# Kernel optimization log

Measured on AMD Instinct MI355X. Metric: run time of the kernel, lower is better.

## Reference

```python
import jax, jax.numpy as jnp
import numpy as np

N_HEAD = 16
EPS = 1e-6


def setup_inputs() -> dict:
    key = jax.random.key(0)
    ks = jax.random.split(key, 5)
    B, T, C = 2, 2048, 1024
    hd = C // N_HEAD
    x = jax.random.normal(ks[0], (B, T, C), dtype=jnp.float32)
    # rotary frequencies (unit-magnitude complex, decomposed into cos/sin)
    theta = 10000.0 ** (-np.arange(0, hd, 2, dtype=np.float32) / hd)  # [hd/2]
    ang = np.arange(T, dtype=np.float32)[:, None] * theta[None, :]    # [T, hd/2]
    freqs_cos = jnp.asarray(np.cos(ang))
    freqs_sin = jnp.asarray(np.sin(ang))
    w_attn = jax.random.normal(ks[1], (3 * C, C), dtype=jnp.float32) * 0.02
    w_proj = jax.random.normal(ks[2], (C, C), dtype=jnp.float32) * 0.02
    q_norm_w = jnp.ones((hd,), dtype=jnp.float32)
    k_norm_w = jnp.ones((hd,), dtype=jnp.float32)
    return {"x": x, "freqs_cos": freqs_cos, "freqs_sin": freqs_sin,
            "w_attn": w_attn, "w_proj": w_proj,
            "q_norm_w": q_norm_w, "k_norm_w": k_norm_w}


def _rmsnorm(x, w):
    # x: [..., hd]; per-last-dim RMSNorm with learned scale
    rms = jax.lax.rsqrt(jnp.mean(x * x, axis=-1, keepdims=True) + EPS)
    return x * rms * w


def _rope(x, cos, sin):
    # x: [B, T, H, hd]; cos/sin: [T, hd/2] -> broadcast [1, T, 1, hd/2]
    x2 = x.reshape(*x.shape[:-1], -1, 2)  # [B,T,H,hd/2,2]
    x0, x1 = x2[..., 0], x2[..., 1]
    c = cos[None, :, None, :]
    s = sin[None, :, None, :]
    r0 = x0 * c - x1 * s
    r1 = x0 * s + x1 * c
    return jnp.stack([r0, r1], axis=-1).reshape(x.shape)


def reference(x, freqs_cos, freqs_sin, w_attn, w_proj, q_norm_w, k_norm_w):
    B, T, C = x.shape
    H = N_HEAD
    hd = C // H
    qkv = x @ w_attn.T  # [B, T, 3C]
    q, k, v = jnp.split(qkv, 3, axis=-1)
    q = q.reshape(B, T, H, hd)
    k = k.reshape(B, T, H, hd)
    v = v.reshape(B, T, H, hd)
    q = _rmsnorm(q, q_norm_w)
    k = _rmsnorm(k, k_norm_w)
    q = _rope(q, freqs_cos[:T], freqs_sin[:T])
    k = _rope(k, freqs_cos[:T], freqs_sin[:T])
    scale = 1.0 / jnp.sqrt(jnp.asarray(hd, dtype=x.dtype))
    # causal SDPA: scores [B, H, T, T]
    scores = jnp.einsum('bihd,bjhd->bhij', q, k) * scale
    causal = jnp.tril(jnp.ones((T, T), dtype=bool))
    scores = jnp.where(causal[None, None], scores, jnp.finfo(scores.dtype).min)
    p = jax.nn.softmax(scores, axis=-1)
    y = jnp.einsum('bhij,bjhd->bihd', p, v).reshape(B, T, C)
    return y @ w_proj.T
```

## Files before the change

kernel.cpp:

```cpp
#include <hip/hip_runtime.h>

typedef unsigned short u16;
typedef unsigned int u32;
typedef __bf16 bf16x8 __attribute__((ext_vector_type(8)));
typedef float f32x4 __attribute__((ext_vector_type(4)));

__device__ __forceinline__ u16 f2bf(float f) {
    union { float f; u32 u; } v;
    v.f = f;
    u32 r = v.u + 0x7fffu + ((v.u >> 16) & 1u);
    return (u16)(r >> 16);
}

__device__ __forceinline__ u32 fbits(float f) {
    union { float f; u32 u; } v; v.f = f; return v.u;
}

__device__ __forceinline__ void glds16(const void* g, void* l) {
    __builtin_amdgcn_global_load_lds(
        (__attribute__((address_space(1))) unsigned int*)(g),
        (__attribute__((address_space(3))) unsigned int*)(l), 16, 0, 0);
}

#define MFMA __builtin_amdgcn_mfma_f32_16x16x32_bf16

__global__ void castbf3(const float* __restrict__ a, u16* __restrict__ oa,
                        const float* __restrict__ b, u16* __restrict__ ob,
                        const float* __restrict__ c, u16* __restrict__ oc,
                        const float* __restrict__ fcos, const float* __restrict__ fsin,
                        float2* __restrict__ csb) {
    int blk = blockIdx.x;
    if (blk < 4096) {
        int i = blk * 256 + threadIdx.x;
        float4 v = ((const float4*)a)[i];
        ushort4 o;
        o.x = f2bf(v.x); o.y = f2bf(v.y); o.z = f2bf(v.z); o.w = f2bf(v.w);
        ((ushort4*)oa)[i] = o;
    } else if (blk < 7168) {
        int i = (blk - 4096) * 256 + threadIdx.x;
        int n = i >> 8, c4 = i & 255;
        int np;
        if (n < 2048) {
            int part = n >> 10, rem = n & 1023;
            int h = rem >> 6, d = rem & 63;
            int nd = (d >> 1) + ((d & 1) << 5);
            np = part * 1024 + h * 64 + nd;
        } else np = n;
        float4 v = ((const float4*)b)[i];
        ushort4 o;
        o.x = f2bf(v.x); o.y = f2bf(v.y); o.z = f2bf(v.z); o.w = f2bf(v.w);
        ((ushort4*)ob)[np * 256 + c4] = o;
    } else if (blk < 8192) {
        int i = (blk - 7168) * 256 + threadIdx.x;
        float4 v = ((const float4*)c)[i];
        ushort4 o;
        o.x = f2bf(v.x); o.y = f2bf(v.y); o.z = f2bf(v.z); o.w = f2bf(v.w);
        ((ushort4*)oc)[i] = o;
    } else {
        int i = (blk - 8192) * 256 + threadIdx.x;
        csb[i] = make_float2(fcos[i], fsin[i]);
    }
}

__global__ __launch_bounds__(256) void gemm_qkv(
    const u16* __restrict__ A, const u16* __restrict__ B,
    const float2* __restrict__ csb,
    const float* __restrict__ qw, const float* __restrict__ kw,
    u16* __restrict__ q, u16* __restrict__ k, u16* __restrict__ vt)
{
    __shared__ alignas(16) u16 SB[2 * 8192];
    u16* Es = SB;
    const int tid = threadIdx.x;
    const int lane = tid & 63;
    const int wave = tid >> 6;
    const int bm = blockIdx.y * 128, bn = blockIdx.x * 128;
    const int wm = (wave >> 1) * 64, wn = (wave & 1) * 64;
    const int ln = lane & 15, quad = lane >> 4;
    const int K = 1024;

    f32x4 acc[4][4] = {};

    const int srow = tid >> 2;
    const int scol = (tid & 3) * 8;
    const u16* gA = A + (size_t)(bm + srow) * K + scol;
    const u16* gB = B + (size_t)(bn + srow) * K + scol;

    auto stage = [&](int k0, int bf) {
        u16* lA = &SB[bf * 8192 + wave * 512];
        u16* lB = &SB[bf * 8192 + 4096 + wave * 512];
        glds16(gA + k0, lA);
        glds16(gA + (size_t)64 * K + k0, lA + 2048);
        glds16(gB + k0, lB);
        glds16(gB + (size_t)64 * K + k0, lB + 2048);
    };

    stage(0, 0);
    for (int it = 0; it < 32; ++it) {
        stage((((it + 1) & 31) << 5), (it + 1) & 1);
        asm volatile("s_waitcnt vmcnt(4)\n\ts_barrier" ::: "memory");

        const u16* Asb = &SB[(it & 1) * 8192];
        const u16* Bsb = Asb + 4096;
        bf16x8 af[4], bfr[4];
#pragma unroll
        for (int i = 0; i < 4; ++i)
            af[i] = *(const bf16x8*)&Asb[(wm + i * 16 + ln) * 32 + quad * 8];
#pragma unroll
        for (int j = 0; j < 4; ++j)
            bfr[j] = *(const bf16x8*)&Bsb[(wn + j * 16 + ln) * 32 + quad * 8];
#pragma unroll
        for (int i = 0; i < 4; ++i)
#pragma unroll
            for (int j = 0; j < 4; ++j)
                acc[i][j] = MFMA(af[i], bfr[j], acc[i][j], 0, 0, 0);

        asm volatile("s_barrier" ::: "memory");
    }
    asm volatile("s_waitcnt vmcnt(0)\n\ts_barrier" ::: "memory");

    const int part = bn >> 10;
    const int headw = wave & 1;
    const int h0 = (bn & 1023) >> 6;
    const float SC = 0.18033688011112042f;
    const int b = bm >> 11, tbase = bm & 2047;

    if (part == 2) {
#pragma unroll
        for (int i = 0; i < 4; ++i) {
            int tlb = wm + i * 16 + quad * 4;
#pragma unroll
            for (int j = 0; j < 4; ++j) {
                int d = j * 16 + ln;
                uint2 pk;
                pk.x = __builtin_amdgcn_perm(fbits(acc[i][j][1]), fbits(acc[i][j][0]), 0x07060302u);
                pk.y = __builtin_amdgcn_perm(fbits(acc[i][j][3]), fbits(acc[i][j][2]), 0x07060302u);
                *(uint2*)&Es[headw * 8192 + d * 128 + (tlb ^ (ln << 3))] = pk;
            }
        }
        __syncthreads();
#pragma unroll
        for (int c = 0; c < 8; ++c) {
            int cid = c * 256 + tid;
            int tc = cid & 15, d = (cid >> 4) & 63, hd = cid >> 10;
            uint4 v = *(const uint4*)&Es[hd * 8192 + d * 128 + ((tc ^ (d & 15)) << 3)];
            size_t dst = ((size_t)((b * 16 + h0 + hd) * 64 + d)) * 2048
                       + tbase + ((tc >> 3) << 6) + (((tc & 7) ^ (d & 7)) << 3);
            *(uint4*)&vt[dst] = v;
        }
        return;
    }

    const float* nw = (part == 0) ? qw : kw;
    float wv[4];
#pragma unroll
    for (int j = 0; j < 4; ++j) {
        int nd = j * 16 + ln;
        int od = ((nd & 31) << 1) | (nd >> 5);
        wv[j] = nw[od];
    }

    if (part == 0) {
#pragma unroll
        for (int i = 0; i < 4; ++i) {
            float oj[4][4];
#pragma unroll
            for (int r = 0; r < 4; ++r) {
                int tloc = wm + i * 16 + quad * 4 + r;
                int t = (bm + tloc) & 2047;
                float v0 = acc[i][0][r], v1 = acc[i][1][r];
                float v2 = acc[i][2][r], v3 = acc[i][3][r];
                float ss = v0 * v0 + v1 * v1 + v2 * v2 + v3 * v3;
                ss += __shfl_xor(ss, 1);
                ss += __shfl_xor(ss, 2);
                ss += __shfl_xor(ss, 4);
                ss += __shfl_xor(ss, 8);
                float g = rsqrtf(ss * (1.0f / 64.0f) + 1e-6f) * SC;
                float x0a = v0 * g * wv[0], x0b = v1 * g * wv[1];
                float x1a = v2 * g * wv[2], x1b = v3 * g * wv[3];
                float2 cs0 = csb[t * 32 + ln];
                float2 cs1 = csb[t * 32 + 16 + ln];
                oj[0][r] = x0a * cs0.x - x1a * cs0.y;
                oj[2][r] = x0a * cs0.y + x1a * cs0.x;
                oj[1][r] = x0b * cs1.x - x1b * cs1.y;
                oj[3][r] = x0b * cs1.y + x1b * cs1.x;
            }
            int tlb = wm + i * 16 + quad * 4;
#pragma unroll
            for (int j = 0; j < 4; ++j) {
                uint2 pk;
                pk.x = __builtin_amdgcn_perm(fbits(oj[j][1]), fbits(oj[j][0]), 0x07060302u);
                pk.y = __builtin_amdgcn_perm(fbits(oj[j][3]), fbits(oj[j][2]), 0x07060302u);
                *(uint2*)&Es[headw * 8192 + (j * 16 + ln) * 128 + (tlb ^ (ln << 3))] = pk;
            }
        }
        __syncthreads();
#pragma unroll
        for (int c = 0; c < 8; ++c) {
            int cid = c * 256 + tid;
            int tc = cid & 15, d = (cid >> 4) & 63, hd = cid >> 10;
            uint4 v = *(const uint4*)&Es[hd * 8192 + d * 128 + ((tc ^ (d & 15)) << 3)];
            size_t dst = ((size_t)((b * 16 + h0 + hd) * 64 + d)) * 2048 + tbase + tc * 8;
            *(uint4*)&q[dst] = v;
        }
        return;
    }

#pragma unroll
    for (int i = 0; i < 4; ++i) {
#pragma unroll
        for (int r = 0; r < 4; ++r) {
            int tloc = wm + i * 16 + quad * 4 + r;
            int t = (bm + tloc) & 2047;

            float v0 = acc[i][0][r], v1 = acc[i][1][r];
            float v2 = acc[i][2][r], v3 = acc[i][3][r];
            float ss = v0 * v0 + v1 * v1 + v2 * v2 + v3 * v3;
            ss += __shfl_xor(ss, 1);
            ss += __shfl_xor(ss, 2);
            ss += __shfl_xor(ss, 4);
            ss += __shfl_xor(ss, 8);
            float g = rsqrtf(ss * (1.0f / 64.0f) + 1e-6f);

            float x0a = v0 * g * wv[0], x0b = v1 * g * wv[1];
            float x1a = v2 * g * wv[2], x1b = v3 * g * wv[3];
            float2 cs0 = csb[t * 32 + ln];
            float2 cs1 = csb[t * 32 + 16 + ln];
            float o0 = x0a * cs0.x - x1a * cs0.y;
            float o2 = x0a * cs0.y + x1a * cs0.x;
            float o1 = x0b * cs1.x - x1b * cs1.y;
            float o3 = x0b * cs1.y + x1b * cs1.x;

            u16* e = &Es[headw * 8192 + tloc * 64 + ln];
            e[((0 ^ quad) << 4)] = f2bf(o0);
            e[((1 ^ quad) << 4)] = f2bf(o1);
            e[((2 ^ quad) << 4)] = f2bf(o2);
            e[((3 ^ quad) << 4)] = f2bf(o3);
        }
    }
    __syncthreads();
#pragma unroll
    for (int c = 0; c < 8; ++c) {
        int cid = c * 256 + tid;
        int dc = cid & 7, tloc = (cid >> 3) & 127, hd = cid >> 10;
        int q2 = (tloc >> 2) & 3;
        int sq = (dc >> 1) ^ q2;
        uint4 v = *(const uint4*)&Es[hd * 8192 + tloc * 64 + sq * 16 + (dc & 1) * 8];
        int gm = bm + tloc;
        int bb = gm >> 11, t = gm & 2047;
        size_t rb = ((size_t)((bb * 16 + h0 + hd) * 2048 + t)) * 64;
        *(uint4*)&k[rb + ((dc ^ (t & 7)) << 3)] = v;
    }
}

__global__ __launch_bounds__(256) void gemm64(
    const u16* __restrict__ A, const u16* __restrict__ B,
    float* __restrict__ C, int M, int N, int K)
{
    __shared__ alignas(16) u16 SB[2 * 6144];
    const int tid = threadIdx.x;
    const int lane = tid & 63;
    const int wave = tid >> 6;
    const int bm = blockIdx.y * 64, bn = blockIdx.x * 128;
    const int wm = (wave >> 1) * 32, wn = (wave & 1) * 64;
    const int ln = lane & 15, quad = lane >> 4;

    f32x4 acc[2][4] = {};

    const int srow = tid >> 2;
    const int scol = (tid & 3) * 8;
    const u16* gA = A + (size_t)(bm + srow) * K + scol;
    const u16* gB = B + (size_t)(bn + srow) * K + scol;

    auto stage = [&](int k0, int bf) {
        u16* lA = &SB[bf * 6144 + wave * 512];
        u16* lB = &SB[bf * 6144 + 2048 + wave * 512];
        glds16(gA + k0, lA);
        glds16(gB + k0, lB);
        glds16(gB + (size_t)64 * K + k0, lB + 2048);
    };

    stage(0, 0);
    for (int it = 0; it < 32; ++it) {
        stage((((it + 1) & 31) << 5), (it + 1) & 1);
        asm volatile("s_waitcnt vmcnt(3)\n\ts_barrier" ::: "memory");

        const u16* Asb = &SB[(it & 1) * 6144];
        const u16* Bsb = Asb + 2048;
        bf16x8 af[2], bfr[4];
#pragma unroll
        for (int i = 0; i < 2; ++i)
            af[i] = *(const bf16x8*)&Asb[(wm + i * 16 + ln) * 32 + quad * 8];
#pragma unroll
        for (int j = 0; j < 4; ++j)
            bfr[j] = *(const bf16x8*)&Bsb[(wn + j * 16 + ln) * 32 + quad * 8];
#pragma unroll
        for (int i = 0; i < 2; ++i)
#pragma unroll
            for (int j = 0; j < 4; ++j)
                acc[i][j] = MFMA(af[i], bfr[j], acc[i][j], 0, 0, 0);

        asm volatile("s_barrier" ::: "memory");
    }

#pragma unroll
    for (int i = 0; i < 2; ++i) {
#pragma unroll
        for (int r = 0; r < 4; ++r) {
            int gm = bm + wm + i * 16 + quad * 4 + r;
            float* Crow = C + (size_t)gm * N + bn + wn + ln;
#pragma unroll
            for (int j = 0; j < 4; ++j)
                Crow[j * 16] = acc[i][j][r];
        }
    }
}

__global__ __launch_bounds__(512) void attn_kernel(
    const u16* __restrict__ Q, const u16* __restrict__ K,
    const u16* __restrict__ VT, u16* __restrict__ Y)
{
    __shared__ alignas(16) u16 Ks[2][64 * 64];
    __shared__ alignas(16) u16 Vs[2][64 * 64];
    __shared__ alignas(16) u16 Ps[8][16 * 80];

    const int tid = threadIdx.x;
    const int lane = tid & 63;
    const int wave = tid >> 6;
    const int ln = lane & 15, quad = lane >> 4;
    const int pi = blockIdx.x;
    const int bh = blockIdx.y;
    const int qaIdx = pi, qbIdx = 31 - pi;
    const bool isB = wave >= 4;
    const int qidx = isB ? qbIdx : qaIdx;
    const int myq = qidx * 64 + (wave & 3) * 16;
    const size_t base = (size_t)bh * 2048 * 64;
    const u16* Kg = K + base;
    const u16* Vg = VT + base;
    const __bf16* Qg = (const __bf16*)(Q + base);

    const int qt = myq + ln;
    bf16x8 qf0, qf1;
#pragma unroll
    for (int j = 0; j < 8; ++j) {
        qf0[j] = Qg[(size_t)(quad * 8 + j) * 2048 + qt];
        qf1[j] = Qg[(size_t)(32 + quad * 8 + j) * 2048 + qt];
    }

    f32x4 o[4] = {};
    float l = 0.0f;
    const int nstages = qbIdx + 1;
    const int sw = ln & 7;
    const int srow = wave * 8 + (lane >> 3);
    const int scol = (lane & 7) * 8;
    u16* Psw = &Ps[wave][0];

    auto prefetch = [&](int jb, int nb) {
        glds16(&Kg[(size_t)(jb + srow) * 64 + scol], &Ks[nb][wave * 512]);
        glds16(&Vg[(size_t)srow * 2048 + jb + scol], &Vs[nb][wave * 512]);
    };
    auto computeS = [&](f32x4* st, const u16* ksb) {
#pragma unroll
        for (int ct = 0; ct < 4; ++ct) {
            bf16x8 kf0 = *(const bf16x8*)&ksb[(ct * 16 + ln) * 64 + (quad ^ sw) * 8];
            bf16x8 kf1 = *(const bf16x8*)&ksb[(ct * 16 + ln) * 64 + ((4 + quad) ^ sw) * 8];
            f32x4 z = {};
            z = MFMA(kf0, qf0, z, 0, 0, 0);
            st[ct] = MFMA(kf1, qf1, z, 0, 0, 0);
        }
    };
    auto applyMask = [&](f32x4* st, int jb) {
        const int qg = myq + ln;
#pragma unroll
        for (int ct = 0; ct < 4; ++ct)
#pragma unroll
            for (int r = 0; r < 4; ++r)
                if (jb + ct * 16 + quad * 4 + r > qg) st[ct][r] = -1e30f;
    };

    prefetch(0, 0);
    asm volatile("s_waitcnt vmcnt(0)\n\ts_barrier" ::: "memory");
    f32x4 st[4];
    computeS(st, &Ks[0][0]);
    if (qidx == 0) applyMask(st, 0);

    for (int jt = 0; jt < nstages; ++jt) {
        const bool haveNext = (jt + 1 < nstages);
        if (haveNext) prefetch((jt + 1) * 64, (jt + 1) & 1);

        const bool curActive = isB || jt <= qaIdx;
        if (curActive) {
            float sum = 0.0f;
#pragma unroll
            for (int ct = 0; ct < 4; ++ct) {
                float e0 = exp2f(st[ct][0]), e1 = exp2f(st[ct][1]);
                float e2 = exp2f(st[ct][2]), e3 = exp2f(st[ct][3]);
                sum += (e0 + e1) + (e2 + e3);
                uint2 pk;
                pk.x = __builtin_amdgcn_perm(fbits(e1), fbits(e0), 0x07060302u);
                pk.y = __builtin_amdgcn_perm(fbits(e3), fbits(e2), 0x07060302u);
                *(uint2*)&Psw[ln * 80 + ct * 16 + quad * 4] = pk;
            }
            l += sum;
        }

        asm volatile("s_waitcnt vmcnt(0)\n\ts_barrier" ::: "memory");

        const bool nextActive = haveNext && (isB || (jt + 1) <= qaIdx);
        if (nextActive) {
            computeS(st, &Ks[(jt + 1) & 1][0]);
            if (jt + 1 == qidx) applyMask(st, (jt + 1) * 64);
        }

        if (curActive) {
            __builtin_amdgcn_s_waitcnt(0xC07F);
            bf16x8 pf0 = *(const bf16x8*)&Psw[ln * 80 + quad * 8];
            bf16x8 pf1 = *(const bf16x8*)&Psw[ln * 80 + 32 + quad * 8];
            const u16* vsb = &Vs[jt & 1][0];
#pragma unroll
            for (int dt = 0; dt < 4; ++dt) {
                bf16x8 vf0 = *(const bf16x8*)&vsb[(dt * 16 + ln) * 64 + (quad ^ sw) * 8];
                bf16x8 vf1 = *(const bf16x8*)&vsb[(dt * 16 + ln) * 64 + ((4 + quad) ^ sw) * 8];
                o[dt] = MFMA(pf0, vf0, o[dt], 0, 0, 0);
                o[dt] = MFMA(pf1, vf1, o[dt], 0, 0, 0);
            }
        }
        asm volatile("s_waitcnt lgkmcnt(0)\n\ts_barrier" ::: "memory");
    }

    l += __shfl_xor(l, 16);
    l += __shfl_xor(l, 32);

    const int b = bh >> 4, h = bh & 15;
#pragma unroll
    for (int r = 0; r < 4; ++r) {
        float lr = __shfl(l, (lane & 48) + quad * 4 + r);
        float inv = 1.0f / lr;
        int gq = myq + quad * 4 + r;
        size_t yb = ((size_t)(b * 2048 + gq)) * 1024 + h * 64 + ln;
#pragma unroll
        for (int dt = 0; dt < 4; ++dt)
            Y[yb + dt * 16] = f2bf(o[dt][r] * inv);
    }
}

extern "C" void kernel_launch(void* const* d_in, const int* in_sizes, int n_in,
                              void* d_out, int out_size, void* d_ws, size_t ws_size,
                              hipStream_t stream) {
    const float* x      = (const float*)d_in[0];
    const float* fcos   = (const float*)d_in[1];
    const float* fsin   = (const float*)d_in[2];
    const float* w_attn = (const float*)d_in[3];
    const float* w_proj = (const float*)d_in[4];
    const float* qw     = (const float*)d_in[5];
    const float* kw     = (const float*)d_in[6];
    float* out = (float*)d_out;

    char* ws = (char*)d_ws;
    u16*    xb  = (u16*)(ws + 0);
    u16*    yb  = (u16*)(ws + 0);
    u16*    wab = (u16*)(ws + 8388608);
    u16*    wpb = (u16*)(ws + 14680064);
    u16*    qb  = (u16*)(ws + 16777216);
    u16*    kb  = (u16*)(ws + 25165824);
    u16*    vtb = (u16*)(ws + 33554432);
    float2* csb = (float2*)(ws + 41943040);

    castbf3<<<8448, 256, 0, stream>>>(x, xb, w_attn, wab, w_proj, wpb, fcos, fsin, csb);

    gemm_qkv<<<dim3(24, 32), 256, 0, stream>>>(xb, wab, csb, qw, kw, qb, kb, vtb);

    attn_kernel<<<dim3(16, 32), 512, 0, stream>>>(qb, kb, vtb, yb);

    gemm64<<<dim3(8, 64), 256, 0, stream>>>(yb, wpb, out, 4096, 1024, 1024);
}
```

Measured before the change: 187.6 us.

## Give each attention wave two 16-row query tiles, halve block size, add setprio

The attention block shrinks from 8 to 4 waves, and each wave now handles 32 query rows as two 16-row sub-tiles. Each K and V fragment read from LDS is therefore reused across two MFMA sets, which halves LDS fragment traffic per unit of compute. Each wave now issues four global-to-LDS loads per stage instead of two. The MFMA sections are wrapped in s_setprio to favour matrix issue. Costs are higher register pressure (doubled accumulators, scores and Q fragments) and fewer waves per block to hide latency.

Measured after the change: 213.2 us. 13.7% more time.

```diff
diff --git a/kernel.cpp b/kernel.cpp
--- a/kernel.cpp
+++ b/kernel.cpp
@@ -315,13 +315,13 @@
     }
 }
 
-__global__ __launch_bounds__(512) void attn_kernel(
+__global__ __launch_bounds__(256) void attn_kernel(
     const u16* __restrict__ Q, const u16* __restrict__ K,
     const u16* __restrict__ VT, u16* __restrict__ Y)
 {
     __shared__ alignas(16) u16 Ks[2][64 * 64];
     __shared__ alignas(16) u16 Vs[2][64 * 64];
-    __shared__ alignas(16) u16 Ps[8][16 * 80];
+    __shared__ alignas(16) u16 Ps[4][2][16 * 80];
 
     const int tid = threadIdx.x;
     const int lane = tid & 63;
@@ -330,58 +330,69 @@
     const int pi = blockIdx.x;
     const int bh = blockIdx.y;
     const int qaIdx = pi, qbIdx = 31 - pi;
-    const bool isB = wave >= 4;
+    const bool isB = wave >= 2;
     const int qidx = isB ? qbIdx : qaIdx;
-    const int myq = qidx * 64 + (wave & 3) * 16;
+    const int myq = qidx * 64 + (wave & 1) * 32;
     const size_t base = (size_t)bh * 2048 * 64;
     const u16* Kg = K + base;
     const u16* Vg = VT + base;
     const __bf16* Qg = (const __bf16*)(Q + base);
 
-    const int qt = myq + ln;
-    bf16x8 qf0, qf1;
-#pragma unroll
-    for (int j = 0; j < 8; ++j) {
-        qf0[j] = Qg[(size_t)(quad * 8 + j) * 2048 + qt];
-        qf1[j] = Qg[(size_t)(32 + quad * 8 + j) * 2048 + qt];
-    }
-
-    f32x4 o[4] = {};
-    float l = 0.0f;
+    bf16x8 qf[2][2];
+#pragma unroll
+    for (int m = 0; m < 2; ++m) {
+        const int qt = myq + m * 16 + ln;
+#pragma unroll
+        for (int j = 0; j < 8; ++j) {
+            qf[m][0][j] = Qg[(size_t)(quad * 8 + j) * 2048 + qt];
+            qf[m][1][j] = Qg[(size_t)(32 + quad * 8 + j) * 2048 + qt];
+        }
+    }
+
+    f32x4 o[2][4] = {};
+    float l[2] = {0.0f, 0.0f};
     const int nstages = qbIdx + 1;
     const int sw = ln & 7;
-    const int srow = wave * 8 + (lane >> 3);
-    const int scol = (lane & 7) * 8;
-    u16* Psw = &Ps[wave][0];
+    const int r8 = lane >> 3;
+    const int c8 = (lane & 7) * 8;
 
     auto prefetch = [&](int jb, int nb) {
-        glds16(&Kg[(size_t)(jb + srow) * 64 + scol], &Ks[nb][wave * 512]);
-        glds16(&Vg[(size_t)srow * 2048 + jb + scol], &Vs[nb][wave * 512]);
+        glds16(&Kg[(size_t)(jb + wave * 16 + r8) * 64 + c8], &Ks[nb][wave * 1024]);
+        glds16(&Kg[(size_t)(jb + wave * 16 + 8 + r8) * 64 + c8], &Ks[nb][wave * 1024 + 512]);
+        glds16(&Vg[(size_t)(wave * 16 + r8) * 2048 + jb + c8], &Vs[nb][wave * 1024]);
+        glds16(&Vg[(size_t)(wave * 16 + 8 + r8) * 2048 + jb + c8], &Vs[nb][wave * 1024 + 512]);
     };
-    auto computeS = [&](f32x4* st, const u16* ksb) {
+
+    f32x4 st[2][4];
+    auto computeS = [&](const u16* ksb) {
 #pragma unroll
         for (int ct = 0; ct < 4; ++ct) {
             bf16x8 kf0 = *(const bf16x8*)&ksb[(ct * 16 + ln) * 64 + (quad ^ sw) * 8];
             bf16x8 kf1 = *(const bf16x8*)&ksb[(ct * 16 + ln) * 64 + ((4 + quad) ^ sw) * 8];
-            f32x4 z = {};
-            z = MFMA(kf0, qf0, z, 0, 0, 0);
-            st[ct] = MFMA(kf1, qf1, z, 0, 0, 0);
+#pragma unroll
+            for (int m = 0; m < 2; ++m) {
+                f32x4 z = {};
+                z = MFMA(kf0, qf[m][0], z, 0, 0, 0);
+                st[m][ct] = MFMA(kf1, qf[m][1], z, 0, 0, 0);
+            }
         }
     };
-    auto applyMask = [&](f32x4* st, int jb) {
-        const int qg = myq + ln;
-#pragma unroll
-        for (int ct = 0; ct < 4; ++ct)
-#pragma unroll
-            for (int r = 0; r < 4; ++r)
-                if (jb + ct * 16 + quad * 4 + r > qg) st[ct][r] = -1e30f;
+    auto applyMask = [&](int jb) {
+#pragma unroll
+        for (int m = 0; m < 2; ++m) {
+            const int qg = myq + m * 16 + ln;
+#pragma unroll
+            for (int ct = 0; ct < 4; ++ct)
+#pragma unroll
+                for (int r = 0; r < 4; ++r)
+                    if (jb + ct * 16 + quad * 4 + r > qg) st[m][ct][r] = -1e30f;
+        }
     };
 
     prefetch(0, 0);
     asm volatile("s_waitcnt vmcnt(0)\n\ts_barrier" ::: "memory");
-    f32x4 st[4];
-    computeS(st, &Ks[0][0]);
-    if (qidx == 0) applyMask(st, 0);
+    computeS(&Ks[0][0]);
+    if (qidx == 0) applyMask(0);
 
     for (int jt = 0; jt < nstages; ++jt) {
         const bool haveNext = (jt + 1 < nstages);
@@ -389,57 +400,75 @@
 
         const bool curActive = isB || jt <= qaIdx;
         if (curActive) {
-            float sum = 0.0f;
-#pragma unroll
-            for (int ct = 0; ct < 4; ++ct) {
-                float e0 = exp2f(st[ct][0]), e1 = exp2f(st[ct][1]);
-                float e2 = exp2f(st[ct][2]), e3 = exp2f(st[ct][3]);
-                sum += (e0 + e1) + (e2 + e3);
-                uint2 pk;
-                pk.x = __builtin_amdgcn_perm(fbits(e1), fbits(e0), 0x07060302u);
-                pk.y = __builtin_amdgcn_perm(fbits(e3), fbits(e2), 0x07060302u);
-                *(uint2*)&Psw[ln * 80 + ct * 16 + quad * 4] = pk;
-            }
-            l += sum;
+#pragma unroll
+            for (int m = 0; m < 2; ++m) {
+                float sum = 0.0f;
+                u16* Psw = &Ps[wave][m][0];
+#pragma unroll
+                for (int ct = 0; ct < 4; ++ct) {
+                    float e0 = exp2f(st[m][ct][0]), e1 = exp2f(st[m][ct][1]);
+                    float e2 = exp2f(st[m][ct][2]), e3 = exp2f(st[m][ct][3]);
+                    sum += (e0 + e1) + (e2 + e3);
+                    uint2 pk;
+                    pk.x = __builtin_amdgcn_perm(fbits(e1), fbits(e0), 0x07060302u);
+                    pk.y = __builtin_amdgcn_perm(fbits(e3), fbits(e2), 0x07060302u);
+                    *(uint2*)&Psw[ln * 80 + ct * 16 + quad * 4] = pk;
+                }
+                l[m] += sum;
+            }
         }
 
         asm volatile("s_waitcnt vmcnt(0)\n\ts_barrier" ::: "memory");
 
         const bool nextActive = haveNext && (isB || (jt + 1) <= qaIdx);
         if (nextActive) {
-            computeS(st, &Ks[(jt + 1) & 1][0]);
-            if (jt + 1 == qidx) applyMask(st, (jt + 1) * 64);
+            __builtin_amdgcn_s_setprio(1);
+            computeS(&Ks[(jt + 1) & 1][0]);
+            __builtin_amdgcn_s_setprio(0);
+            if (jt + 1 == qidx) applyMask((jt + 1) * 64);
         }
 
         if (curActive) {
             __builtin_amdgcn_s_waitcnt(0xC07F);
-            bf16x8 pf0 = *(const bf16x8*)&Psw[ln * 80 + quad * 8];
-            bf16x8 pf1 = *(const bf16x8*)&Psw[ln * 80 + 32 + quad * 8];
+            bf16x8 pf[2][2];
+#pragma unroll
+            for (int m = 0; m < 2; ++m) {
+                pf[m][0] = *(const bf16x8*)&Ps[wave][m][ln * 80 + quad * 8];
+                pf[m][1] = *(const bf16x8*)&Ps[wave][m][ln * 80 + 32 + quad * 8];
+            }
             const u16* vsb = &Vs[jt & 1][0];
+            __builtin_amdgcn_s_setprio(1);
 #pragma unroll
             for (int dt = 0; dt < 4; ++dt) {
                 bf16x8 vf0 = *(const bf16x8*)&vsb[(dt * 16 + ln) * 64 + (quad ^ sw) * 8];
                 bf16x8 vf1 = *(const bf16x8*)&vsb[(dt * 16 + ln) * 64 + ((4 + quad) ^ sw) * 8];
-                o[dt] = MFMA(pf0, vf0, o[dt], 0, 0, 0);
-                o[dt] = MFMA(pf1, vf1, o[dt], 0, 0, 0);
-            }
+#pragma unroll
+                for (int m = 0; m < 2; ++m) {
+                    o[m][dt] = MFMA(pf[m][0], vf0, o[m][dt], 0, 0, 0);
+                    o[m][dt] = MFMA(pf[m][1], vf1, o[m][dt], 0, 0, 0);
+                }
+            }
+            __builtin_amdgcn_s_setprio(0);
         }
         asm volatile("s_waitcnt lgkmcnt(0)\n\ts_barrier" ::: "memory");
     }
 
-    l += __shfl_xor(l, 16);
-    l += __shfl_xor(l, 32);
-
     const int b = bh >> 4, h = bh & 15;
 #pragma unroll
-    for (int r = 0; r < 4; ++r) {
-        float lr = __shfl(l, (lane & 48) + quad * 4 + r);
-        float inv = 1.0f / lr;
-        int gq = myq + quad * 4 + r;
-        size_t yb = ((size_t)(b * 2048 + gq)) * 1024 + h * 64 + ln;
-#pragma unroll
-        for (int dt = 0; dt < 4; ++dt)
-            Y[yb + dt * 16] = f2bf(o[dt][r] * inv);
+    for (int m = 0; m < 2; ++m) {
+        float lm = l[m];
+        lm += __shfl_xor(lm, 16);
+        lm += __shfl_xor(lm, 32);
+#pragma unroll
+        for (int r = 0; r < 4; ++r) {
+            float lr = __shfl(lm, (lane & 48) + quad * 4 + r);
+            float inv = 1.0f / lr;
+            int gq = myq + m * 16 + quad * 4 + r;
+            size_t yb = ((size_t)(b * 2048 + gq)) * 1024 + h * 64 + ln;
+#pragma unroll
+            for (int dt = 0; dt < 4; ++dt)
+                Y[yb + dt * 16] = f2bf(o[m][dt][r] * inv);
+        }
     }
 }
 
@@ -469,7 +498,7 @@
 
     gemm_qkv<<<dim3(24, 32), 256, 0, stream>>>(xb, wab, csb, qw, kw, qb, kb, vtb);
 
-    attn_kernel<<<dim3(16, 32), 512, 0, stream>>>(qb, kb, vtb, yb);
+    attn_kernel<<<dim3(16, 32), 256, 0, stream>>>(qb, kb, vtb, yb);
 
     gemm64<<<dim3(8, 64), 256, 0, stream>>>(yb, wpb, out, 4096, 1024, 1024);
 }
```

## Triple-buffer GEMM K-loop staging and raise wave priority around attention MFMAs

Applied to the files above, without the earlier changes.

Both GEMM kernels move from double to triple buffering of the LDS tiles, prefetching two K-steps ahead with adjusted vmcnt waits, so global loads have more time in flight before they are consumed. The old wrap-around dummy load is removed and the tail iterations drain outstanding loads explicitly. The attention kernel wraps its QK and PV MFMA sections in s_setprio(1)/s_setprio(0) so MFMA-issuing waves get scheduling priority over softmax work in other waves. Triple buffering increases LDS use per block, which may reduce occupancy.

After: 186.4 us. About the same (-0.7%).

```diff
diff --git a/kernel.cpp b/kernel.cpp
--- a/kernel.cpp
+++ b/kernel.cpp
@@ -68,7 +68,7 @@
     const float* __restrict__ qw, const float* __restrict__ kw,
     u16* __restrict__ q, u16* __restrict__ k, u16* __restrict__ vt)
 {
-    __shared__ alignas(16) u16 SB[2 * 8192];
+    __shared__ alignas(16) u16 SB[3 * 8192];
     u16* Es = SB;
     const int tid = threadIdx.x;
     const int lane = tid & 63;
@@ -95,11 +95,19 @@
     };
 
     stage(0, 0);
+    stage(32, 1);
+    int cb = 0, nb = 2;
     for (int it = 0; it < 32; ++it) {
-        stage((((it + 1) & 31) << 5), (it + 1) & 1);
-        asm volatile("s_waitcnt vmcnt(4)\n\ts_barrier" ::: "memory");
-
-        const u16* Asb = &SB[(it & 1) * 8192];
+        if (it < 30) {
+            stage((it + 2) << 5, nb);
+            asm volatile("s_waitcnt vmcnt(8)\n\ts_barrier" ::: "memory");
+        } else if (it == 30) {
+            asm volatile("s_waitcnt vmcnt(4)\n\ts_barrier" ::: "memory");
+        } else {
+            asm volatile("s_waitcnt vmcnt(0)\n\ts_barrier" ::: "memory");
+        }
+
+        const u16* Asb = &SB[cb * 8192];
         const u16* Bsb = Asb + 4096;
         bf16x8 af[4], bfr[4];
 #pragma unroll
@@ -115,8 +123,9 @@
                 acc[i][j] = MFMA(af[i], bfr[j], acc[i][j], 0, 0, 0);
 
         asm volatile("s_barrier" ::: "memory");
-    }
-    asm volatile("s_waitcnt vmcnt(0)\n\ts_barrier" ::: "memory");
+        cb = (cb == 2) ? 0 : cb + 1;
+        nb = (nb == 2) ? 0 : nb + 1;
+    }
 
     const int part = bn >> 10;
     const int headw = wave & 1;
@@ -256,7 +265,7 @@
     const u16* __restrict__ A, const u16* __restrict__ B,
     float* __restrict__ C, int M, int N, int K)
 {
-    __shared__ alignas(16) u16 SB[2 * 6144];
+    __shared__ alignas(16) u16 SB[3 * 6144];
     const int tid = threadIdx.x;
     const int lane = tid & 63;
     const int wave = tid >> 6;
@@ -280,11 +289,19 @@
     };
 
     stage(0, 0);
+    stage(32, 1);
+    int cb = 0, nb = 2;
     for (int it = 0; it < 32; ++it) {
-        stage((((it + 1) & 31) << 5), (it + 1) & 1);
-        asm volatile("s_waitcnt vmcnt(3)\n\ts_barrier" ::: "memory");
-
-        const u16* Asb = &SB[(it & 1) * 6144];
+        if (it < 30) {
+            stage((it + 2) << 5, nb);
+            asm volatile("s_waitcnt vmcnt(6)\n\ts_barrier" ::: "memory");
+        } else if (it == 30) {
+            asm volatile("s_waitcnt vmcnt(3)\n\ts_barrier" ::: "memory");
+        } else {
+            asm volatile("s_waitcnt vmcnt(0)\n\ts_barrier" ::: "memory");
+        }
+
+        const u16* Asb = &SB[cb * 6144];
         const u16* Bsb = Asb + 2048;
         bf16x8 af[2], bfr[4];
 #pragma unroll
@@ -300,6 +317,8 @@
                 acc[i][j] = MFMA(af[i], bfr[j], acc[i][j], 0, 0, 0);
 
         asm volatile("s_barrier" ::: "memory");
+        cb = (cb == 2) ? 0 : cb + 1;
+        nb = (nb == 2) ? 0 : nb + 1;
     }
 
 #pragma unroll
@@ -407,7 +426,9 @@
 
         const bool nextActive = haveNext && (isB || (jt + 1) <= qaIdx);
         if (nextActive) {
+            __builtin_amdgcn_s_setprio(1);
             computeS(st, &Ks[(jt + 1) & 1][0]);
+            __builtin_amdgcn_s_setprio(0);
             if (jt + 1 == qidx) applyMask(st, (jt + 1) * 64);
         }
 
@@ -416,6 +437,7 @@
             bf16x8 pf0 = *(const bf16x8*)&Psw[ln * 80 + quad * 8];
             bf16x8 pf1 = *(const bf16x8*)&Psw[ln * 80 + 32 + quad * 8];
             const u16* vsb = &Vs[jt & 1][0];
+            __builtin_amdgcn_s_setprio(1);
 #pragma unroll
             for (int dt = 0; dt < 4; ++dt) {
                 bf16x8 vf0 = *(const bf16x8*)&vsb[(dt * 16 + ln) * 64 + (quad ^ sw) * 8];
@@ -423,6 +445,7 @@
                 o[dt] = MFMA(pf0, vf0, o[dt], 0, 0, 0);
                 o[dt] = MFMA(pf1, vf1, o[dt], 0, 0, 0);
             }
+            __builtin_amdgcn_s_setprio(0);
         }
         asm volatile("s_waitcnt lgkmcnt(0)\n\ts_barrier" ::: "memory");
     }
```
